# Optimization experiments

Measured on AMD Instinct MI355X. Metric: run time of the kernel, lower is better.

## Reference

```python
import jax, jax.numpy as jnp
import numpy as np

H = 1024        # hidden_dim
MD = 2048       # memory_dim
L = 16384       # memory length == max_length
N = 8           # head_N
# sys.float_info.min underflows to 0.0 in float32, exactly as in the torch
# original (python float * float32 tensor). Kept for faithfulness.
TINY = jnp.float32(2.2250738585072014e-308)


def setup_inputs() -> dict:
    key = jax.random.key(0)
    ks = jax.random.split(key, 12)
    s_h = 1.0 / np.sqrt(H)
    s_m = 1.0 / np.sqrt(MD)
    s_o = 1.0 / np.sqrt(2 * H)
    return {
        "x": jax.random.normal(ks[0], (1, 1, H), jnp.float32),
        "memory": jax.random.normal(ks[1], (L, MD), jnp.float32),
        "Wq": jax.random.uniform(ks[2], (H, H), jnp.float32, -s_h, s_h),
        "bq": jax.random.uniform(ks[3], (H,), jnp.float32, -s_h, s_h),
        "Wk": jax.random.uniform(ks[4], (H, MD), jnp.float32, -s_m, s_m),
        "bk": jax.random.uniform(ks[5], (H,), jnp.float32, -s_m, s_m),
        "Wv": jax.random.uniform(ks[6], (H, MD), jnp.float32, -s_m, s_m),
        "bv": jax.random.uniform(ks[7], (H,), jnp.float32, -s_m, s_m),
        "Wo": jax.random.uniform(ks[8], (H, 2 * H), jnp.float32, -s_o, s_o),
        "bo": jax.random.uniform(ks[9], (H,), jnp.float32, -s_o, s_o),
    }


def reference(x, memory, Wq, bq, Wk, bk, Wv, bv, Wo, bo):
    d = H // N  # per-head dim
    # Q: (1,H) -> (1,d,N) -> (N,1,d), scaled by d**-0.5
    q = x.reshape(1, -1) @ Wq.T + bq
    Q = q.reshape(1, d, N).transpose(2, 0, 1) * (d ** -0.5)
    # K: (L,H) -> (L,d,N) -> (N,d,L)
    K = (memory @ Wk.T + bk).reshape(-1, d, N).transpose(2, 1, 0)
    QK = jnp.einsum('nod,ndl->nol', Q, K)  # (N,1,L)
    # pad mask: 1 where the memory row sums to zero, else 0 (as in torch nonzero-set)
    any_zero = memory.sum(axis=1)
    pad_mask = (any_zero == 0).astype(QK.dtype)[None, None, :]
    QK = QK + pad_mask * TINY
    attn = jax.nn.softmax(QK, axis=-1)
    # V: (L,H) -> (L,d,N) -> (N,L,d)
    V = (memory @ Wv.T + bv).reshape(-1, d, N).transpose(2, 0, 1)
    feat = jnp.einsum('nol,nld->nod', attn, V)      # (N,1,d)
    feat = feat.transpose(1, 2, 0).reshape(1, 1, H)  # (1,1,H)
    ax = jnp.concatenate([x, feat], axis=-1)         # (1,1,2H)
    return jax.nn.relu(ax @ Wo.T + bo)
```

## Files before the change

kernel.cpp:

```cpp
#include <hip/hip_runtime.h>
#include <math.h>

#define LROWS 16384
#define HDIM  1024
#define MDIM  2048
#define NH    8
#define RSQRT_D 0.08838834764831844f

#define OFF_W     0
#define OFF_BETA  16384
#define OFF_Z     16392
#define OFF_Q     16400
#define OFF_FEAT  17424
#define OFF_Y     18448
#define OFF_YBUF  34832

__device__ __forceinline__ float dot4(float4 a, float4 b) {
  return a.x * b.x + a.y * b.y + a.z * b.z + a.w * b.w;
}
__device__ __forceinline__ void fma4(float4& acc, float s, float4 v) {
  acc.x = fmaf(s, v.x, acc.x); acc.y = fmaf(s, v.y, acc.y);
  acc.z = fmaf(s, v.z, acc.z); acc.w = fmaf(s, v.w, acc.w);
}
__device__ __forceinline__ void add4(float4& a, float4 v) {
  a.x += v.x; a.y += v.y; a.z += v.z; a.w += v.w;
}

__global__ __launch_bounds__(256) void k1_q(const float* __restrict__ x,
                                            const float* __restrict__ Wq,
                                            const float* __restrict__ bq,
                                            const float* __restrict__ bk,
                                            float* __restrict__ ws) {
  int tid = threadIdx.x, lane = tid & 63;
  int j = blockIdx.x * 4 + (tid >> 6);
  const float4* xr = (const float4*)x;
  const float4* wr = (const float4*)(Wq + (size_t)j * HDIM);
  float acc = 0.f;
#pragma unroll
  for (int i = 0; i < 4; ++i) {
    int idx = i * 64 + lane;
    acc += dot4(xr[idx], wr[idx]);
  }
#pragma unroll
  for (int off = 32; off; off >>= 1) acc += __shfl_xor(acc, off);
  if (lane == 0) {
    float qj = acc + bq[j];
    ws[OFF_Q + j] = qj;
    atomicAdd(&ws[OFF_BETA + (j & 7)], qj * bk[j]);
  }
}

__global__ __launch_bounds__(256) void k2_w(const float* __restrict__ Wk,
                                            float* __restrict__ ws) {
  int tid = threadIdx.x;
  int mc = blockIdx.x & 7, cc = blockIdx.x >> 3;
  int m = mc * 256 + tid;
  const float* q = ws + OFF_Q;
  float acc[8];
#pragma unroll
  for (int n = 0; n < 8; ++n) acc[n] = 0.f;
  int c0 = cc * 64;
  for (int c = c0; c < c0 + 64; c += 8) {
#pragma unroll
    for (int u = 0; u < 8; ++u)
      acc[u] = fmaf(q[c + u], Wk[(size_t)(c + u) * MDIM + m], acc[u]);
  }
#pragma unroll
  for (int n = 0; n < 8; ++n) atomicAdd(&ws[OFF_W + n * MDIM + m], acc[n]);
}

__global__ __launch_bounds__(256, 2) void k35(const float* __restrict__ mem,
                                              float* __restrict__ ws) {
  __shared__ float sred[4 * 32 * 33];
  __shared__ float4 pv4[32];
  int tid = threadIdx.x, lane = tid & 63, wv = tid >> 6;
  const float* wmat = ws + OFF_W;
  float* pv = (float*)pv4;

  float4 y0[8], y1[8];
#pragma unroll
  for (int n = 0; n < 8; ++n) {
    y0[n] = make_float4(0.f, 0.f, 0.f, 0.f);
    y1[n] = make_float4(0.f, 0.f, 0.f, 0.f);
  }
  float zacc = 0.f;

  for (int g = 0; g < 2; ++g) {
    int r0 = blockIdx.x * 32 + g * 16;
    float acc[4][8];
#pragma unroll
    for (int rr = 0; rr < 4; ++rr)
#pragma unroll
      for (int n = 0; n < 8; ++n) acc[rr][n] = 0.f;
    for (int step = 0; step < 8; ++step) {
      int mq = step * 64 + lane;
      float4 wvv[8];
#pragma unroll
      for (int n = 0; n < 8; ++n)
        wvv[n] = *(const float4*)(wmat + n * MDIM + mq * 4);
#pragma unroll
      for (int rr = 0; rr < 4; ++rr) {
        float4 mv = *(const float4*)(mem + (size_t)(r0 + wv * 4 + rr) * MDIM + mq * 4);
#pragma unroll
        for (int n = 0; n < 8; ++n) {
          acc[rr][n] = fmaf(mv.x, wvv[n].x, acc[rr][n]);
          acc[rr][n] = fmaf(mv.y, wvv[n].y, acc[rr][n]);
          acc[rr][n] = fmaf(mv.z, wvv[n].z, acc[rr][n]);
          acc[rr][n] = fmaf(mv.w, wvv[n].w, acc[rr][n]);
        }
      }
    }
#pragma unroll
    for (int rr = 0; rr < 4; ++rr)
#pragma unroll
      for (int n = 0; n < 8; ++n) acc[rr][n] += __shfl_xor(acc[rr][n], 32);
    if (lane < 32) {
#pragma unroll
      for (int rr = 0; rr < 4; ++rr)
#pragma unroll
        for (int n = 0; n < 8; ++n)
          sred[wv * 1056 + lane * 33 + rr * 8 + n] = acc[rr][n];
    }
    __syncthreads();
    if (tid < 128) {
      int rowl = tid >> 3, n = tid & 7;
      int wvx = rowl >> 2, rr = rowl & 3;
      const float* base = sred + wvx * 1056 + rr * 8 + n;
      float s = 0.f;
#pragma unroll
      for (int l = 0; l < 32; ++l) s += base[l * 33];
      s = (s + ws[OFF_BETA + n]) * RSQRT_D;
      float p = __expf(s);
      pv[rowl * 8 + n] = p;
      zacc += p;
    }
    __syncthreads();
#pragma unroll 4
    for (int rl = 0; rl < 16; ++rl) {
      const float* row = mem + (size_t)(r0 + rl) * MDIM;
      float4 m0 = *(const float4*)(row + tid * 4);
      float4 m1 = *(const float4*)(row + 1024 + tid * 4);
      float4 pA = pv4[rl * 2];
      float4 pB = pv4[rl * 2 + 1];
      fma4(y0[0], pA.x, m0); fma4(y1[0], pA.x, m1);
      fma4(y0[1], pA.y, m0); fma4(y1[1], pA.y, m1);
      fma4(y0[2], pA.z, m0); fma4(y1[2], pA.z, m1);
      fma4(y0[3], pA.w, m0); fma4(y1[3], pA.w, m1);
      fma4(y0[4], pB.x, m0); fma4(y1[4], pB.x, m1);
      fma4(y0[5], pB.y, m0); fma4(y1[5], pB.y, m1);
      fma4(y0[6], pB.z, m0); fma4(y1[6], pB.z, m1);
      fma4(y0[7], pB.w, m0); fma4(y1[7], pB.w, m1);
    }
    __syncthreads();
  }
  float* yb = ws + OFF_YBUF + (size_t)blockIdx.x * 16384;
#pragma unroll
  for (int n = 0; n < 8; ++n) {
    *(float4*)(yb + n * MDIM + tid * 4) = y0[n];
    *(float4*)(yb + n * MDIM + 1024 + tid * 4) = y1[n];
  }
  if (tid < 128) {
    float z = zacc;
    z += __shfl_xor(z, 8); z += __shfl_xor(z, 16); z += __shfl_xor(z, 32);
    if ((tid & 63) < 8) atomicAdd(&ws[OFF_Z + (tid & 7)], z);
  }
}

__global__ __launch_bounds__(256) void k4c(float* __restrict__ ws) {
  __shared__ float4 sA[256];
  int t = threadIdx.x;
  int quad = blockIdx.x * 16 + (t & 15);
  int b0 = (t >> 4) * 32;
  const float4* src = (const float4*)(ws + OFF_YBUF);
  float4 acc = make_float4(0.f, 0.f, 0.f, 0.f);
  for (int b = b0; b < b0 + 32; ++b)
    add4(acc, src[(size_t)b * 4096 + quad]);
  sA[(t & 15) * 16 + (t >> 4)] = acc;
  __syncthreads();
  if (t < 16) {
    float4 s = sA[t * 16];
#pragma unroll
    for (int j = 1; j < 16; ++j) add4(s, sA[t * 16 + j]);
    ((float4*)(ws + OFF_Y))[blockIdx.x * 16 + t] = s;
  }
}

__global__ __launch_bounds__(256) void k6_feat(const float* __restrict__ Wv,
                                               const float* __restrict__ bv,
                                               float* __restrict__ ws) {
  int tid = threadIdx.x, lane = tid & 63;
  int c = blockIdx.x * 4 + (tid >> 6);
  int n = c & 7;
  const float4* yb = (const float4*)(ws + OFF_Y + n * MDIM);
  const float4* wb = (const float4*)(Wv + (size_t)c * MDIM);
  float acc = 0.f;
#pragma unroll
  for (int s = 0; s < 8; ++s) {
    int idx = s * 64 + lane;
    acc += dot4(yb[idx], wb[idx]);
  }
#pragma unroll
  for (int off = 32; off; off >>= 1) acc += __shfl_xor(acc, off);
  if (lane == 0) ws[OFF_FEAT + c] = acc / ws[OFF_Z + n] + bv[c];
}

__global__ __launch_bounds__(256) void k7_out(const float* __restrict__ x,
                                              const float* __restrict__ Wo,
                                              const float* __restrict__ bo,
                                              const float* __restrict__ ws,
                                              float* __restrict__ out) {
  int tid = threadIdx.x, lane = tid & 63;
  int j = blockIdx.x * 4 + (tid >> 6);
  const float4* wb = (const float4*)(Wo + (size_t)j * 2048);
  const float4* xr = (const float4*)x;
  const float4* fr = (const float4*)(ws + OFF_FEAT);
  float acc = 0.f;
#pragma unroll
  for (int s = 0; s < 4; ++s) {
    int idx = s * 64 + lane;
    acc += dot4(xr[idx], wb[idx]);
    acc += dot4(fr[idx], wb[256 + idx]);
  }
#pragma unroll
  for (int off = 32; off; off >>= 1) acc += __shfl_xor(acc, off);
  if (lane == 0) out[j] = fmaxf(acc + bo[j], 0.f);
}

extern "C" void kernel_launch(void* const* d_in, const int* in_sizes, int n_in,
                              void* d_out, int out_size, void* d_ws, size_t ws_size,
                              hipStream_t stream) {
  const float* x   = (const float*)d_in[0];
  const float* mem = (const float*)d_in[1];
  const float* Wq  = (const float*)d_in[2];
  const float* bq  = (const float*)d_in[3];
  const float* Wk  = (const float*)d_in[4];
  const float* bk  = (const float*)d_in[5];
  const float* Wv  = (const float*)d_in[6];
  const float* bv  = (const float*)d_in[7];
  const float* Wo  = (const float*)d_in[8];
  const float* bo  = (const float*)d_in[9];
  float* ws  = (float*)d_ws;
  float* out = (float*)d_out;

  hipMemsetAsync(ws, 0, OFF_Q * sizeof(float), stream);

  k1_q   <<<256, 256, 0, stream>>>(x, Wq, bq, bk, ws);
  k2_w   <<<128, 256, 0, stream>>>(Wk, ws);
  k35    <<<512, 256, 0, stream>>>(mem, ws);
  k4c    <<<256, 256, 0, stream>>>(ws);
  k6_feat<<<256, 256, 0, stream>>>(Wv, bv, ws);
  k7_out <<<256, 256, 0, stream>>>(x, Wo, bo, ws, out);
}
```

Measured before the change: 301.5 us.

## Split fused score/weighted-sum kernel into separate score and weighted-sum kernels

The fused k35 kernel, which computed exp scores and then the p-weighted sum of memory rows per block, is split into two kernels. kA_scores writes per-row probabilities to a workspace buffer and accumulates Z, and kB_wsum reads them back to build the per-block weighted sums over half-width column chunks. The intent is more blocks, fewer registers per kernel and higher occupancy (launch bounds raised to 4 waves per SIMD). In exchange, the 128 MB memory matrix is read twice from global memory (or L2/MALL) instead of once per block, and an extra launch is added.

```diff
diff --git a/kernel.cpp b/kernel.cpp
--- a/kernel.cpp
+++ b/kernel.cpp
@@ -13,7 +13,8 @@
 #define OFF_Q     16400
 #define OFF_FEAT  17424
 #define OFF_Y     18448
-#define OFF_YBUF  34832
+#define OFF_P     34832
+#define OFF_YBUF  165904
 
 __device__ __forceinline__ float dot4(float4 a, float4 b) {
   return a.x * b.x + a.y * b.y + a.z * b.z + a.w * b.w;
@@ -69,101 +70,96 @@
   for (int n = 0; n < 8; ++n) atomicAdd(&ws[OFF_W + n * MDIM + m], acc[n]);
 }
 
-__global__ __launch_bounds__(256, 2) void k35(const float* __restrict__ mem,
-                                              float* __restrict__ ws) {
+__global__ __launch_bounds__(256, 4) void kA_scores(const float* __restrict__ mem,
+                                                    float* __restrict__ ws) {
   __shared__ float sred[4 * 32 * 33];
-  __shared__ float4 pv4[32];
   int tid = threadIdx.x, lane = tid & 63, wv = tid >> 6;
   const float* wmat = ws + OFF_W;
-  float* pv = (float*)pv4;
-
-  float4 y0[8], y1[8];
-#pragma unroll
-  for (int n = 0; n < 8; ++n) {
-    y0[n] = make_float4(0.f, 0.f, 0.f, 0.f);
-    y1[n] = make_float4(0.f, 0.f, 0.f, 0.f);
-  }
-  float zacc = 0.f;
-
-  for (int g = 0; g < 2; ++g) {
-    int r0 = blockIdx.x * 32 + g * 16;
-    float acc[4][8];
+  int r0 = blockIdx.x * 16;
+
+  float acc[4][8];
+#pragma unroll
+  for (int rr = 0; rr < 4; ++rr)
+#pragma unroll
+    for (int n = 0; n < 8; ++n) acc[rr][n] = 0.f;
+
+  for (int step = 0; step < 8; ++step) {
+    int mq = step * 64 + lane;
+    float4 mv[4];
 #pragma unroll
     for (int rr = 0; rr < 4; ++rr)
-#pragma unroll
-      for (int n = 0; n < 8; ++n) acc[rr][n] = 0.f;
-    for (int step = 0; step < 8; ++step) {
-      int mq = step * 64 + lane;
-      float4 wvv[8];
-#pragma unroll
-      for (int n = 0; n < 8; ++n)
-        wvv[n] = *(const float4*)(wmat + n * MDIM + mq * 4);
-#pragma unroll
-      for (int rr = 0; rr < 4; ++rr) {
-        float4 mv = *(const float4*)(mem + (size_t)(r0 + wv * 4 + rr) * MDIM + mq * 4);
-#pragma unroll
-        for (int n = 0; n < 8; ++n) {
-          acc[rr][n] = fmaf(mv.x, wvv[n].x, acc[rr][n]);
-          acc[rr][n] = fmaf(mv.y, wvv[n].y, acc[rr][n]);
-          acc[rr][n] = fmaf(mv.z, wvv[n].z, acc[rr][n]);
-          acc[rr][n] = fmaf(mv.w, wvv[n].w, acc[rr][n]);
-        }
+      mv[rr] = *(const float4*)(mem + (size_t)(r0 + wv * 4 + rr) * MDIM + mq * 4);
+    float4 wvv[8];
+#pragma unroll
+    for (int n = 0; n < 8; ++n)
+      wvv[n] = *(const float4*)(wmat + n * MDIM + mq * 4);
+#pragma unroll
+    for (int rr = 0; rr < 4; ++rr) {
+#pragma unroll
+      for (int n = 0; n < 8; ++n) {
+        acc[rr][n] = fmaf(mv[rr].x, wvv[n].x, acc[rr][n]);
+        acc[rr][n] = fmaf(mv[rr].y, wvv[n].y, acc[rr][n]);
+        acc[rr][n] = fmaf(mv[rr].z, wvv[n].z, acc[rr][n]);
+        acc[rr][n] = fmaf(mv[rr].w, wvv[n].w, acc[rr][n]);
       }
     }
+  }
+#pragma unroll
+  for (int rr = 0; rr < 4; ++rr)
+#pragma unroll
+    for (int n = 0; n < 8; ++n) acc[rr][n] += __shfl_xor(acc[rr][n], 32);
+  if (lane < 32) {
 #pragma unroll
     for (int rr = 0; rr < 4; ++rr)
 #pragma unroll
-      for (int n = 0; n < 8; ++n) acc[rr][n] += __shfl_xor(acc[rr][n], 32);
-    if (lane < 32) {
-#pragma unroll
-      for (int rr = 0; rr < 4; ++rr)
-#pragma unroll
-        for (int n = 0; n < 8; ++n)
-          sred[wv * 1056 + lane * 33 + rr * 8 + n] = acc[rr][n];
-    }
-    __syncthreads();
-    if (tid < 128) {
-      int rowl = tid >> 3, n = tid & 7;
-      int wvx = rowl >> 2, rr = rowl & 3;
-      const float* base = sred + wvx * 1056 + rr * 8 + n;
-      float s = 0.f;
-#pragma unroll
-      for (int l = 0; l < 32; ++l) s += base[l * 33];
-      s = (s + ws[OFF_BETA + n]) * RSQRT_D;
-      float p = __expf(s);
-      pv[rowl * 8 + n] = p;
-      zacc += p;
-    }
-    __syncthreads();
+      for (int n = 0; n < 8; ++n)
+        sred[wv * 1056 + lane * 33 + rr * 8 + n] = acc[rr][n];
+  }
+  __syncthreads();
+  if (tid < 128) {
+    int rowl = tid >> 3, n = tid & 7;
+    int wvx = rowl >> 2, rr = rowl & 3;
+    const float* base = sred + wvx * 1056 + rr * 8 + n;
+    float s = 0.f;
+#pragma unroll
+    for (int l = 0; l < 32; ++l) s += base[l * 33];
+    s = (s + ws[OFF_BETA + n]) * RSQRT_D;
+    float p = __expf(s);
+    ws[OFF_P + (size_t)(r0 + rowl) * 8 + n] = p;
+    float z = p;
+    z += __shfl_xor(z, 8); z += __shfl_xor(z, 16); z += __shfl_xor(z, 32);
+    if ((tid & 63) < 8) atomicAdd(&ws[OFF_Z + n], z);
+  }
+}
+
+__global__ __launch_bounds__(256, 4) void kB_wsum(const float* __restrict__ mem,
+                                                  float* __restrict__ ws) {
+  __shared__ float pp[32 * 8];
+  int tid = threadIdx.x;
+  int rc = blockIdx.x >> 1, ch = blockIdx.x & 1;
+  int r0 = rc * 32;
+  pp[tid] = ws[OFF_P + (size_t)r0 * 8 + tid];
+  __syncthreads();
+
+  float4 acc[8];
+#pragma unroll
+  for (int n = 0; n < 8; ++n) acc[n] = make_float4(0.f, 0.f, 0.f, 0.f);
+
+  const float* base = mem + (size_t)r0 * MDIM + ch * 1024 + tid * 4;
 #pragma unroll 4
-    for (int rl = 0; rl < 16; ++rl) {
-      const float* row = mem + (size_t)(r0 + rl) * MDIM;
-      float4 m0 = *(const float4*)(row + tid * 4);
-      float4 m1 = *(const float4*)(row + 1024 + tid * 4);
-      float4 pA = pv4[rl * 2];
-      float4 pB = pv4[rl * 2 + 1];
-      fma4(y0[0], pA.x, m0); fma4(y1[0], pA.x, m1);
-      fma4(y0[1], pA.y, m0); fma4(y1[1], pA.y, m1);
-      fma4(y0[2], pA.z, m0); fma4(y1[2], pA.z, m1);
-      fma4(y0[3], pA.w, m0); fma4(y1[3], pA.w, m1);
-      fma4(y0[4], pB.x, m0); fma4(y1[4], pB.x, m1);
-      fma4(y0[5], pB.y, m0); fma4(y1[5], pB.y, m1);
-      fma4(y0[6], pB.z, m0); fma4(y1[6], pB.z, m1);
-      fma4(y0[7], pB.w, m0); fma4(y1[7], pB.w, m1);
-    }
-    __syncthreads();
-  }
-  float* yb = ws + OFF_YBUF + (size_t)blockIdx.x * 16384;
-#pragma unroll
-  for (int n = 0; n < 8; ++n) {
-    *(float4*)(yb + n * MDIM + tid * 4) = y0[n];
-    *(float4*)(yb + n * MDIM + 1024 + tid * 4) = y1[n];
-  }
-  if (tid < 128) {
-    float z = zacc;
-    z += __shfl_xor(z, 8); z += __shfl_xor(z, 16); z += __shfl_xor(z, 32);
-    if ((tid & 63) < 8) atomicAdd(&ws[OFF_Z + (tid & 7)], z);
-  }
+  for (int r = 0; r < 32; ++r) {
+    float4 mv = *(const float4*)(base + (size_t)r * MDIM);
+    float4 pA = *(const float4*)(pp + r * 8);
+    float4 pB = *(const float4*)(pp + r * 8 + 4);
+    fma4(acc[0], pA.x, mv); fma4(acc[1], pA.y, mv);
+    fma4(acc[2], pA.z, mv); fma4(acc[3], pA.w, mv);
+    fma4(acc[4], pB.x, mv); fma4(acc[5], pB.y, mv);
+    fma4(acc[6], pB.z, mv); fma4(acc[7], pB.w, mv);
+  }
+  float* yb = ws + OFF_YBUF + (size_t)rc * 16384 + ch * 1024 + tid * 4;
+#pragma unroll
+  for (int n = 0; n < 8; ++n)
+    *(float4*)(yb + n * MDIM) = acc[n];
 }
 
 __global__ __launch_bounds__(256) void k4c(float* __restrict__ ws) {
@@ -244,10 +240,11 @@
 
   hipMemsetAsync(ws, 0, OFF_Q * sizeof(float), stream);
 
-  k1_q   <<<256, 256, 0, stream>>>(x, Wq, bq, bk, ws);
-  k2_w   <<<128, 256, 0, stream>>>(Wk, ws);
-  k35    <<<512, 256, 0, stream>>>(mem, ws);
-  k4c    <<<256, 256, 0, stream>>>(ws);
-  k6_feat<<<256, 256, 0, stream>>>(Wv, bv, ws);
-  k7_out <<<256, 256, 0, stream>>>(x, Wo, bo, ws, out);
-}
+  k1_q    <<<256, 256, 0, stream>>>(x, Wq, bq, bk, ws);
+  k2_w    <<<128, 256, 0, stream>>>(Wk, ws);
+  kA_scores<<<1024, 256, 0, stream>>>(mem, ws);
+  kB_wsum <<<1024, 256, 0, stream>>>(mem, ws);
+  k4c     <<<256, 256, 0, stream>>>(ws);
+  k6_feat <<<256, 256, 0, stream>>>(Wv, bv, ws);
+  k7_out  <<<256, 256, 0, stream>>>(x, Wo, bo, ws, out);
+}
```

After: 336.3 us. 11.5% more time.
